# Kernel optimization log

Hardware: AMD Instinct MI355X
Metric: run time of the kernel (lower is better)

The kernel has to match this reference:

```python
import jax, jax.numpy as jnp
import numpy as np

B, C, H, W = 4, 256, 64, 64
HID = C // 2


def setup_inputs() -> dict:
    key = jax.random.key(0)
    kx, kp, kt, kg, km = jax.random.split(key, 5)
    return {
        "x": jax.random.normal(kx, (B, C, H, W), dtype=jnp.float32),
        "w_phi": jax.random.normal(kp, (HID, C), dtype=jnp.float32) * 0.02,
        "w_theta": jax.random.normal(kt, (HID, C), dtype=jnp.float32) * 0.02,
        "w_g": jax.random.normal(kg, (HID, C), dtype=jnp.float32) * 0.02,
        "w_mask": jax.random.normal(km, (C, HID), dtype=jnp.float32) * 0.02,
    }


def reference(x, w_phi, w_theta, w_g, w_mask):
    b, c, h, w = x.shape
    n = h * w
    xf = x.reshape(b, c, n)                     # [B,C,N]
    # 1x1 convs == channel GEMMs
    phi = jnp.einsum('oc,bcn->bon', w_phi, xf)      # [B,HID,N]
    theta = jnp.einsum('oc,bcn->bon', w_theta, xf)  # [B,HID,N]
    g = jnp.einsum('oc,bcn->bon', w_g, xf)          # [B,HID,N]
    # attn[b,n,m] = sum_c theta[b,c,n] * phi[b,c,m]   (theta^T @ phi)
    attn = jnp.einsum('bcn,bcm->bnm', theta, phi)   # [B,N,N]
    # Faithful to nn.Softmax(dim=1): normalize over axis 1 (theta index)
    attn = jax.nn.softmax(attn, axis=1)
    # attn_g[b,n,c] = sum_m attn[b,n,m] * g[b,c,m]   (attn @ g^T)
    attn_g = jnp.einsum('bnm,bcm->bcn', attn, g)    # [B,HID,N] (already transposed back)
    mask = jnp.einsum('oc,bcn->bon', w_mask, attn_g).reshape(b, c, h, w)
    return mask + x
```

## Files before the change

kernel.cpp:

```cpp
#include <hip/hip_runtime.h>


#define NB   4
#define CIN  256
#define HIDN 128
#define NPIX 4096

typedef __attribute__((ext_vector_type(8))) short short8;
typedef __attribute__((ext_vector_type(4))) float f32x4;
typedef __attribute__((ext_vector_type(16))) float f32x16;

__device__ __forceinline__ unsigned short f2bf(float f) {
    unsigned u = __builtin_bit_cast(unsigned, f);
    u += 0x7fffu + ((u >> 16) & 1u);
    return (unsigned short)(u >> 16);
}
__device__ __forceinline__ unsigned f2bf2(float lo, float hi) {
    return (unsigned)f2bf(lo) | ((unsigned)f2bf(hi) << 16);
}
__device__ __forceinline__ float bf2f(unsigned short s) {
    return __builtin_bit_cast(float, (unsigned)s << 16);
}
__device__ __forceinline__ void cp16(void* lds, const void* g) {
    __builtin_amdgcn_global_load_lds(
        (const __attribute__((address_space(1))) unsigned int*)g,
        (__attribute__((address_space(3))) unsigned int*)lds, 16, 0, 0);
}

__global__ __launch_bounds__(256) void k_proj(
    const float* __restrict__ x,
    const float* __restrict__ w_phi,
    const float* __restrict__ w_theta,
    const float* __restrict__ w_g,
    unsigned short* __restrict__ phiT,
    unsigned short* __restrict__ thetaT,
    unsigned short* __restrict__ gbuf)
{
    const int nt = blockIdx.x, p = blockIdx.y, b = blockIdx.z;
    const int n0 = nt * 128;
    const float* W = (p == 0) ? w_phi : (p == 1) ? w_theta : w_g;
    const float* X = x + (size_t)b * CIN * NPIX;

    __shared__ alignas(16) unsigned short Ws[128][40];
    __shared__ alignas(16) unsigned short Xs[128][40];

    const int tid = threadIdx.x;
    const int wave = tid >> 6, lane = tid & 63;
    const int wm = wave >> 1, wn = wave & 1;
    const int quad = lane >> 4, l16 = lane & 15;

    f32x4 acc[4][4];
#pragma unroll
    for (int i = 0; i < 4; ++i)
#pragma unroll
        for (int j = 0; j < 4; ++j) acc[i][j] = {0.f, 0.f, 0.f, 0.f};

    for (int ks = 0; ks < CIN / 32; ++ks) {
        {
            const int row = tid >> 1, c0 = (tid & 1) * 16;
            const float* src = W + (size_t)row * CIN + ks * 32 + c0;
            unsigned* dst = (unsigned*)&Ws[row][c0];
#pragma unroll
            for (int j = 0; j < 8; ++j) dst[j] = f2bf2(src[2 * j], src[2 * j + 1]);
        }
        {
            const int cp = (tid >> 4) * 2, nn0 = (tid & 15) * 8;
            const float* s0 = X + (size_t)(ks * 32 + cp) * NPIX + n0 + nn0;
            const float* s1 = s0 + NPIX;
#pragma unroll
            for (int j = 0; j < 8; ++j)
                *(unsigned*)&Xs[nn0 + j][cp] = f2bf2(s0[j], s1[j]);
        }
        __syncthreads();
#pragma unroll
        for (int mi = 0; mi < 4; ++mi) {
            short8 a = *(const short8*)&Ws[wm * 64 + mi * 16 + l16][quad * 8];
#pragma unroll
            for (int ni = 0; ni < 4; ++ni) {
                short8 bb = *(const short8*)&Xs[wn * 64 + ni * 16 + l16][quad * 8];
                acc[mi][ni] = __builtin_amdgcn_mfma_f32_16x16x32_bf16(a, bb, acc[mi][ni], 0, 0, 0);
            }
        }
        __syncthreads();
    }

    if (p < 2) {
        unsigned short* T = (p == 0) ? phiT : thetaT;
#pragma unroll
        for (int mi = 0; mi < 4; ++mi) {
            const int obase = wm * 64 + mi * 16 + quad * 4;
#pragma unroll
            for (int ni = 0; ni < 4; ++ni) {
                const int nn = wn * 64 + ni * 16 + l16;
                const int scol = (((obase >> 3) ^ (nn & 15)) << 3) | (obase & 7);
                uint2 v;
                v.x = f2bf2(acc[mi][ni][0], acc[mi][ni][1]);
                v.y = f2bf2(acc[mi][ni][2], acc[mi][ni][3]);
                *(uint2*)&T[((size_t)b * NPIX + n0 + nn) * HIDN + scol] = v;
            }
        }
    } else {
#pragma unroll
        for (int mi = 0; mi < 4; ++mi) {
            const int obase = wm * 64 + mi * 16 + quad * 4;
#pragma unroll
            for (int ni = 0; ni < 4; ++ni) {
                const int nn = wn * 64 + ni * 16 + l16;
#pragma unroll
                for (int r = 0; r < 4; ++r) {
                    const int c = obase + r;
                    const int scol = n0 + ((((nn >> 3) ^ (c & 15)) << 3) | (nn & 7));
                    gbuf[((size_t)b * HIDN + c) * NPIX + scol] = f2bf(acc[mi][ni][r]);
                }
            }
        }
    }
}

__global__ __launch_bounds__(256, 2) void k_colsum(
    const unsigned short* __restrict__ thetaT,
    const unsigned short* __restrict__ phiT,
    float* __restrict__ colsum)
{
    const int mt = blockIdx.x, ntg = blockIdx.y, b = blockIdx.z;
    const int m0 = mt * 128;
    __shared__ alignas(16) unsigned short As[128][128];
    __shared__ alignas(16) unsigned short Bs[128][128];
    const int tid = threadIdx.x;
    const int wave = tid >> 6, lane = tid & 63;
    const int wm = wave >> 1, wn = wave & 1;
    const int quad = lane >> 4, l16 = lane & 15;

    {
        const unsigned short* src = phiT + ((size_t)b * NPIX + m0) * HIDN;
#pragma unroll
        for (int i = 0; i < 8; ++i) {
            const int u = i * 256 + tid;
            cp16(&Bs[0][0] + u * 8, src + u * 8);
        }
    }

    float csum[4] = {0.f, 0.f, 0.f, 0.f};

    for (int nc = 0; nc < 4; ++nc) {
        const int n0 = ntg * 512 + nc * 128;
        __syncthreads();
        {
            const unsigned short* src = thetaT + ((size_t)b * NPIX + n0) * HIDN;
#pragma unroll
            for (int i = 0; i < 8; ++i) {
                const int u = i * 256 + tid;
                cp16(&As[0][0] + u * 8, src + u * 8);
            }
        }
        __syncthreads();

        f32x4 acc[4][4];
#pragma unroll
        for (int i = 0; i < 4; ++i)
#pragma unroll
            for (int j = 0; j < 4; ++j) acc[i][j] = {0.f, 0.f, 0.f, 0.f};

#pragma unroll
        for (int ks = 0; ks < 4; ++ks) {
            const int sc = (((ks * 4 + quad) ^ l16) << 3);
            short8 af[4], bf[4];
#pragma unroll
            for (int mi = 0; mi < 4; ++mi)
                af[mi] = *(const short8*)&As[wm * 64 + mi * 16 + l16][sc];
#pragma unroll
            for (int ni = 0; ni < 4; ++ni)
                bf[ni] = *(const short8*)&Bs[wn * 64 + ni * 16 + l16][sc];
#pragma unroll
            for (int mi = 0; mi < 4; ++mi)
#pragma unroll
                for (int ni = 0; ni < 4; ++ni)
                    acc[mi][ni] = __builtin_amdgcn_mfma_f32_16x16x32_bf16(af[mi], bf[ni], acc[mi][ni], 0, 0, 0);
        }
#pragma unroll
        for (int ni = 0; ni < 4; ++ni)
#pragma unroll
            for (int mi = 0; mi < 4; ++mi)
#pragma unroll
                for (int r = 0; r < 4; ++r) csum[ni] += __expf(acc[mi][ni][r]);
    }

#pragma unroll
    for (int ni = 0; ni < 4; ++ni) {
        float s = csum[ni];
        s += __shfl_xor(s, 16);
        s += __shfl_xor(s, 32);
        if (quad == 0)
            atomicAdd(&colsum[(size_t)b * NPIX + m0 + wn * 64 + ni * 16 + l16], s);
    }
}

__global__ void k_zero(float* __restrict__ p) { p[blockIdx.x * 256 + threadIdx.x] = 0.f; }
__global__ void k_zero4(float* __restrict__ p) {
    const size_t i = (size_t)(blockIdx.x * 256 + threadIdx.x) * 4;
    *(f32x4*)&p[i] = f32x4{0.f, 0.f, 0.f, 0.f};
}

__global__ __launch_bounds__(256) void k_scale_g(
    unsigned short* __restrict__ gbuf, const float* __restrict__ colsum)
{
    const int idx = blockIdx.x * 256 + threadIdx.x;
    const int row = idx >> 9;
    const int sc = (idx & 511) * 8;
    const int bb = row >> 7;
    const int mt = (sc & ~127) | ((((sc >> 3) & 15) ^ (row & 15)) << 3);
    uint4 v = *(uint4*)&gbuf[(size_t)row * NPIX + sc];
    float4 c0 = *(const float4*)&colsum[(size_t)bb * NPIX + mt];
    float4 c1 = *(const float4*)&colsum[(size_t)bb * NPIX + mt + 4];
    unsigned short* vs = (unsigned short*)&v;
    const float cs[8] = {c0.x, c0.y, c0.z, c0.w, c1.x, c1.y, c1.z, c1.w};
#pragma unroll
    for (int j = 0; j < 8; ++j) vs[j] = f2bf(bf2f(vs[j]) / cs[j]);
    *(uint4*)&gbuf[(size_t)row * NPIX + sc] = v;
}

__global__ __launch_bounds__(256, 2) void k_attn(
    const unsigned short* __restrict__ thetaT,
    const unsigned short* __restrict__ phiT,
    const unsigned short* __restrict__ gbuf,
    float* __restrict__ O32)
{
    const int nt = blockIdx.x, ms = blockIdx.y, b = blockIdx.z;
    const int n0 = nt * 64;

    __shared__ alignas(16) unsigned short Bs[128][128];
    __shared__ alignas(16) unsigned short Gs[128][128];
    __shared__ alignas(16) unsigned short Ps[64][128];

    const int tid = threadIdx.x;
    const int wave = tid >> 6, lane = tid & 63;
    const int wm = wave >> 1, wn = wave & 1;
    const int l31 = lane & 31, lh = lane >> 5;
    const int key = l31 & 15;

    short8 afrag[8];
    {
        const int n = n0 + wm * 32 + l31;
        const unsigned short* src = thetaT + ((size_t)b * NPIX + n) * HIDN;
#pragma unroll
        for (int ks = 0; ks < 8; ++ks)
            afrag[ks] = *(const short8*)(src + (((ks * 2 + lh) ^ key) << 3));
    }

    f32x16 accO[2];
#pragma unroll
    for (int r = 0; r < 16; ++r) { accO[0][r] = 0.f; accO[1][r] = 0.f; }

    for (int mc = 0; mc < 16; ++mc) {
        const int m0 = (ms * 16 + mc) * 128;
        __syncthreads();
        {
            const unsigned short* src = phiT + ((size_t)b * NPIX + m0) * HIDN;
#pragma unroll
            for (int i = 0; i < 8; ++i) {
                const int u = i * 256 + tid;
                cp16(&Bs[0][0] + u * 8, src + u * 8);
            }
        }
        {
#pragma unroll
            for (int i = 0; i < 8; ++i) {
                const int u = i * 256 + tid;
                const int row = u >> 4, un = u & 15;
                cp16(&Gs[0][0] + u * 8,
                     gbuf + ((size_t)b * HIDN + row) * NPIX + m0 + un * 8);
            }
        }
        __syncthreads();

        f32x16 accS[2];
#pragma unroll
        for (int r = 0; r < 16; ++r) { accS[0][r] = 0.f; accS[1][r] = 0.f; }
#pragma unroll
        for (int ks = 0; ks < 8; ++ks) {
            const int sc = ((ks * 2 + lh) ^ key) << 3;
            short8 b0 = *(const short8*)&Bs[wn * 64 + l31][sc];
            short8 b1 = *(const short8*)&Bs[wn * 64 + 32 + l31][sc];
            accS[0] = __builtin_amdgcn_mfma_f32_32x32x16_bf16(afrag[ks], b0, accS[0], 0, 0, 0);
            accS[1] = __builtin_amdgcn_mfma_f32_32x32x16_bf16(afrag[ks], b1, accS[1], 0, 0, 0);
        }
#pragma unroll
        for (int ni = 0; ni < 2; ++ni) {
            const int m_loc = wn * 64 + ni * 32 + l31;
#pragma unroll
            for (int r = 0; r < 16; ++r) {
                const int n_loc = wm * 32 + (r & 3) + 8 * (r >> 2) + 4 * lh;
                const int scol = (((m_loc >> 3) ^ (n_loc & 15)) << 3) | (m_loc & 7);
                Ps[n_loc][scol] = f2bf(__expf(accS[ni][r]));
            }
        }
        __syncthreads();
        {
            const int prow = wm * 32 + l31;
            const int pkey = prow & 15;
#pragma unroll
            for (int ks = 0; ks < 8; ++ks) {
                const int sc = ((ks * 2 + lh) ^ key) << 3;
                short8 pa = *(const short8*)&Ps[prow][((ks * 2 + lh) ^ pkey) << 3];
                short8 g0 = *(const short8*)&Gs[wn * 64 + l31][sc];
                short8 g1 = *(const short8*)&Gs[wn * 64 + 32 + l31][sc];
                accO[0] = __builtin_amdgcn_mfma_f32_32x32x16_bf16(pa, g0, accO[0], 0, 0, 0);
                accO[1] = __builtin_amdgcn_mfma_f32_32x32x16_bf16(pa, g1, accO[1], 0, 0, 0);
            }
        }
    }

#pragma unroll
    for (int ni = 0; ni < 2; ++ni)
#pragma unroll
        for (int r = 0; r < 16; ++r) {
            const int n = n0 + wm * 32 + (r & 3) + 8 * (r >> 2) + 4 * lh;
            const int c = wn * 64 + ni * 32 + l31;
            atomicAdd(&O32[((size_t)b * NPIX + n) * HIDN + c], accO[ni][r]);
        }
}

__global__ __launch_bounds__(256) void k_mask(
    const float* __restrict__ w_mask,
    const float* __restrict__ O32,
    const float* __restrict__ x,
    float* __restrict__ out)
{
    const int nt = blockIdx.x, ct = blockIdx.y, b = blockIdx.z;
    const int n0 = nt * 128, c0 = ct * 128;
    __shared__ alignas(16) unsigned short As[128][40];
    __shared__ alignas(16) unsigned short Bs[128][40];
    const int tid = threadIdx.x;
    const int wave = tid >> 6, lane = tid & 63;
    const int wm = wave >> 1, wn = wave & 1;
    const int quad = lane >> 4, l16 = lane & 15;

    f32x4 acc[4][4];
#pragma unroll
    for (int i = 0; i < 4; ++i)
#pragma unroll
        for (int j = 0; j < 4; ++j) acc[i][j] = {0.f, 0.f, 0.f, 0.f};

    for (int ks = 0; ks < 4; ++ks) {
        {
            const int row = tid >> 1, cc0 = (tid & 1) * 16;
            const float* src = w_mask + (size_t)(c0 + row) * HIDN + ks * 32 + cc0;
            unsigned* dst = (unsigned*)&As[row][cc0];
#pragma unroll
            for (int j = 0; j < 8; ++j) dst[j] = f2bf2(src[2 * j], src[2 * j + 1]);
        }
        {
            const int row = tid >> 1, h0 = (tid & 1) * 16;
            const float* src = O32 + ((size_t)b * NPIX + n0 + row) * HIDN + ks * 32 + h0;
            unsigned* dst = (unsigned*)&Bs[row][h0];
#pragma unroll
            for (int j = 0; j < 8; ++j) dst[j] = f2bf2(src[2 * j], src[2 * j + 1]);
        }
        __syncthreads();
#pragma unroll
        for (int mi = 0; mi < 4; ++mi) {
            short8 a = *(const short8*)&As[wm * 64 + mi * 16 + l16][quad * 8];
#pragma unroll
            for (int ni = 0; ni < 4; ++ni) {
                short8 bb = *(const short8*)&Bs[wn * 64 + ni * 16 + l16][quad * 8];
                acc[mi][ni] = __builtin_amdgcn_mfma_f32_16x16x32_bf16(a, bb, acc[mi][ni], 0, 0, 0);
            }
        }
        __syncthreads();
    }

#pragma unroll
    for (int mi = 0; mi < 4; ++mi)
#pragma unroll
        for (int ni = 0; ni < 4; ++ni)
#pragma unroll
            for (int r = 0; r < 4; ++r) {
                const int co = c0 + wm * 64 + mi * 16 + quad * 4 + r;
                const int nn = n0 + wn * 64 + ni * 16 + l16;
                const size_t idx = ((size_t)b * CIN + co) * NPIX + nn;
                out[idx] = acc[mi][ni][r] + x[idx];
            }
}

extern "C" void kernel_launch(void* const* d_in, const int* in_sizes, int n_in,
                              void* d_out, int out_size, void* d_ws, size_t ws_size,
                              hipStream_t stream)
{
    (void)in_sizes; (void)n_in; (void)out_size; (void)ws_size;
    const float* x       = (const float*)d_in[0];
    const float* w_phi   = (const float*)d_in[1];
    const float* w_theta = (const float*)d_in[2];
    const float* w_g     = (const float*)d_in[3];
    const float* w_mask  = (const float*)d_in[4];
    float* out = (float*)d_out;

    char* ws = (char*)d_ws;
    unsigned short* phiT   = (unsigned short*)(ws);
    unsigned short* thetaT = (unsigned short*)(ws + 4194304);
    unsigned short* gbuf   = (unsigned short*)(ws + 8388608);
    float*          colsum = (float*)(ws + 12582912);
    float*          O32    = (float*)(ws + 12648448);

    k_proj   <<<dim3(32, 3, 4), 256, 0, stream>>>(x, w_phi, w_theta, w_g, phiT, thetaT, gbuf);
    k_zero   <<<dim3(64),       256, 0, stream>>>(colsum);
    k_zero4  <<<dim3(2048),     256, 0, stream>>>(O32);
    k_colsum <<<dim3(32, 8, 4), 256, 0, stream>>>(thetaT, phiT, colsum);
    k_scale_g<<<dim3(1024),     256, 0, stream>>>(gbuf, colsum);
    k_attn   <<<dim3(64, 2, 4), 256, 0, stream>>>(thetaT, phiT, gbuf, O32);
    k_mask   <<<dim3(32, 2, 4), 256, 0, stream>>>(w_mask, O32, x, out);
}
```

Baseline: 186.5 us.

## Pre-convert weights and x to swizzled bf16, retile all GEMMs to 32x32 MFMA

Adds prep kernels that convert the weights and a transposed x to bf16 with XOR-swizzled layouts, so the projection and mask GEMMs can stream operands with direct global-to-LDS copies instead of converting fp32 element by element. Zeroing of colsum and O32 moves into the prep and colsum kernels, removing two launches. The projection, colsum, attention and mask kernels are retiled to 32x32x16 MFMA with smaller 64-wide tiles and higher occupancy hints, and attention now uses more blocks over the m dimension. The xT buffer shares workspace space with O32, which O32 only overwrites after xT is consumed. The trade-off is extra launches and global traffic for the prep step, plus more atomics into O32 from the wider split.

Measured after the change: 186.5 us. About the same (-0.0%).

```diff
diff --git a/kernel.cpp b/kernel.cpp
--- a/kernel.cpp
+++ b/kernel.cpp
@@ -27,178 +27,220 @@
         (__attribute__((address_space(3))) unsigned int*)lds, 16, 0, 0);
 }
 
-__global__ __launch_bounds__(256) void k_proj(
+__global__ __launch_bounds__(256) void k_prep_w(
+    const float* __restrict__ wp, const float* __restrict__ wt,
+    const float* __restrict__ wg, const float* __restrict__ wm,
+    unsigned short* __restrict__ Wp, unsigned short* __restrict__ Wt,
+    unsigned short* __restrict__ Wg, unsigned short* __restrict__ Wm)
+{
+    const int which = blockIdx.x >> 3;
+    const float* src = (which == 0) ? wp : (which == 1) ? wt : (which == 2) ? wg : wm;
+    unsigned short* dst = (which == 0) ? Wp : (which == 1) ? Wt : (which == 2) ? Wg : Wm;
+#pragma unroll
+    for (int t = 0; t < 2; ++t) {
+        const int gidx = ((blockIdx.x & 7) * 256 + threadIdx.x) * 2 + t;
+        int o, srcc, dstc;
+        if (which < 3) {
+            o = gidx >> 5;
+            const int gc = gidx & 31;
+            const int sg = (gc & ~15) | ((gc & 15) ^ (o & 15));
+            srcc = o * 256 + gc * 8; dstc = o * 256 + sg * 8;
+        } else {
+            o = gidx >> 4;
+            const int gc = gidx & 15;
+            const int sg = gc ^ (o & 15);
+            srcc = o * 128 + gc * 8; dstc = o * 128 + sg * 8;
+        }
+        float4 a = *(const float4*)&src[srcc];
+        float4 b = *(const float4*)&src[srcc + 4];
+        uint4 v;
+        v.x = f2bf2(a.x, a.y); v.y = f2bf2(a.z, a.w);
+        v.z = f2bf2(b.x, b.y); v.w = f2bf2(b.z, b.w);
+        *(uint4*)&dst[dstc] = v;
+    }
+}
+
+__global__ __launch_bounds__(256) void k_prep_x(
     const float* __restrict__ x,
-    const float* __restrict__ w_phi,
-    const float* __restrict__ w_theta,
-    const float* __restrict__ w_g,
+    unsigned short* __restrict__ xT,
+    float* __restrict__ colsum)
+{
+    const int nt = blockIdx.x, ct = blockIdx.y, b = blockIdx.z;
+    const int tid = threadIdx.x;
+    if (ct == 0 && tid < 64) colsum[(size_t)b * NPIX + nt * 64 + tid] = 0.f;
+
+    __shared__ unsigned short Ls[64][66];
+    {
+        const int c_loc = tid >> 2, n_seg = (tid & 3) * 16;
+        const float* src = x + ((size_t)(b * CIN + ct * 64 + c_loc)) * NPIX + nt * 64 + n_seg;
+#pragma unroll
+        for (int j = 0; j < 8; ++j)
+            *(unsigned*)&Ls[c_loc][n_seg + 2 * j] = f2bf2(src[2 * j], src[2 * j + 1]);
+    }
+    __syncthreads();
+    {
+        const int n_loc = tid >> 2, c_seg = (tid & 3) * 16;
+        const int n_glob = nt * 64 + n_loc;
+        unsigned short tmp[16];
+#pragma unroll
+        for (int j = 0; j < 16; ++j) tmp[j] = Ls[c_seg + j][n_loc];
+#pragma unroll
+        for (int gr = 0; gr < 2; ++gr) {
+            const int c_base = ct * 64 + c_seg + gr * 8;
+            const int sec = c_base >> 7;
+            const int sg = (((c_base >> 3) & 15) ^ (n_glob & 15));
+            *(uint4*)&xT[((size_t)b * NPIX + n_glob) * CIN + sec * 128 + sg * 8] =
+                *(uint4*)&tmp[gr * 8];
+        }
+    }
+}
+
+__global__ __launch_bounds__(256, 3) void k_proj(
+    const unsigned short* __restrict__ Wp,
+    const unsigned short* __restrict__ Wt,
+    const unsigned short* __restrict__ Wg,
+    const unsigned short* __restrict__ xT,
     unsigned short* __restrict__ phiT,
     unsigned short* __restrict__ thetaT,
     unsigned short* __restrict__ gbuf)
 {
-    const int nt = blockIdx.x, p = blockIdx.y, b = blockIdx.z;
-    const int n0 = nt * 128;
-    const float* W = (p == 0) ? w_phi : (p == 1) ? w_theta : w_g;
-    const float* X = x + (size_t)b * CIN * NPIX;
-
-    __shared__ alignas(16) unsigned short Ws[128][40];
-    __shared__ alignas(16) unsigned short Xs[128][40];
+    const int nt = blockIdx.x, ot = blockIdx.y, b = blockIdx.z;
+    const unsigned short* W = (ot == 0) ? Wp : (ot == 1) ? Wt : Wg;
+
+    __shared__ alignas(16) unsigned short Aw[128][128];
+    __shared__ alignas(16) unsigned short Bx[64][128];
 
     const int tid = threadIdx.x;
     const int wave = tid >> 6, lane = tid & 63;
-    const int wm = wave >> 1, wn = wave & 1;
-    const int quad = lane >> 4, l16 = lane & 15;
-
-    f32x4 acc[4][4];
-#pragma unroll
-    for (int i = 0; i < 4; ++i)
-#pragma unroll
-        for (int j = 0; j < 4; ++j) acc[i][j] = {0.f, 0.f, 0.f, 0.f};
-
-    for (int ks = 0; ks < CIN / 32; ++ks) {
-        {
-            const int row = tid >> 1, c0 = (tid & 1) * 16;
-            const float* src = W + (size_t)row * CIN + ks * 32 + c0;
-            unsigned* dst = (unsigned*)&Ws[row][c0];
-#pragma unroll
-            for (int j = 0; j < 8; ++j) dst[j] = f2bf2(src[2 * j], src[2 * j + 1]);
-        }
-        {
-            const int cp = (tid >> 4) * 2, nn0 = (tid & 15) * 8;
-            const float* s0 = X + (size_t)(ks * 32 + cp) * NPIX + n0 + nn0;
-            const float* s1 = s0 + NPIX;
-#pragma unroll
-            for (int j = 0; j < 8; ++j)
-                *(unsigned*)&Xs[nn0 + j][cp] = f2bf2(s0[j], s1[j]);
-        }
-        __syncthreads();
-#pragma unroll
-        for (int mi = 0; mi < 4; ++mi) {
-            short8 a = *(const short8*)&Ws[wm * 64 + mi * 16 + l16][quad * 8];
-#pragma unroll
-            for (int ni = 0; ni < 4; ++ni) {
-                short8 bb = *(const short8*)&Xs[wn * 64 + ni * 16 + l16][quad * 8];
-                acc[mi][ni] = __builtin_amdgcn_mfma_f32_16x16x32_bf16(a, bb, acc[mi][ni], 0, 0, 0);
+    const int oh = wave >> 1, nh = wave & 1;
+    const int l31 = lane & 31, lh = lane >> 5;
+    const int key = l31 & 15;
+
+    f32x16 acc[2];
+#pragma unroll
+    for (int r = 0; r < 16; ++r) { acc[0][r] = 0.f; acc[1][r] = 0.f; }
+
+    for (int kh = 0; kh < 2; ++kh) {
+        __syncthreads();
+#pragma unroll
+        for (int i = 0; i < 8; ++i) {
+            const int u = i * 256 + tid;
+            cp16(&Aw[0][0] + u * 8, W + (u >> 4) * 256 + kh * 128 + (u & 15) * 8);
+        }
+#pragma unroll
+        for (int i = 0; i < 4; ++i) {
+            const int u = i * 256 + tid;
+            cp16(&Bx[0][0] + u * 8,
+                 xT + ((size_t)b * NPIX + nt * 64 + (u >> 4)) * CIN + kh * 128 + (u & 15) * 8);
+        }
+        __syncthreads();
+#pragma unroll
+        for (int ks = 0; ks < 8; ++ks) {
+            const int g = ((ks * 2 + lh) ^ key) << 3;
+            short8 bb = *(const short8*)&Bx[nh * 32 + l31][g];
+#pragma unroll
+            for (int t = 0; t < 2; ++t) {
+                short8 a = *(const short8*)&Aw[oh * 64 + t * 32 + l31][g];
+                acc[t] = __builtin_amdgcn_mfma_f32_32x32x16_bf16(a, bb, acc[t], 0, 0, 0);
             }
         }
-        __syncthreads();
-    }
-
-    if (p < 2) {
-        unsigned short* T = (p == 0) ? phiT : thetaT;
-#pragma unroll
-        for (int mi = 0; mi < 4; ++mi) {
-            const int obase = wm * 64 + mi * 16 + quad * 4;
-#pragma unroll
-            for (int ni = 0; ni < 4; ++ni) {
-                const int nn = wn * 64 + ni * 16 + l16;
-                const int scol = (((obase >> 3) ^ (nn & 15)) << 3) | (obase & 7);
+    }
+
+    const int n_glob = nt * 64 + nh * 32 + l31;
+    if (ot < 2) {
+        unsigned short* T = (ot == 0) ? phiT : thetaT;
+#pragma unroll
+        for (int t = 0; t < 2; ++t)
+#pragma unroll
+            for (int rg = 0; rg < 4; ++rg) {
+                const int ob = oh * 64 + t * 32 + 8 * rg + 4 * lh;
+                const int sc = (((ob >> 3) ^ (n_glob & 15)) << 3) | (ob & 7);
                 uint2 v;
-                v.x = f2bf2(acc[mi][ni][0], acc[mi][ni][1]);
-                v.y = f2bf2(acc[mi][ni][2], acc[mi][ni][3]);
-                *(uint2*)&T[((size_t)b * NPIX + n0 + nn) * HIDN + scol] = v;
+                v.x = f2bf2(acc[t][rg * 4 + 0], acc[t][rg * 4 + 1]);
+                v.y = f2bf2(acc[t][rg * 4 + 2], acc[t][rg * 4 + 3]);
+                *(uint2*)&T[((size_t)b * NPIX + n_glob) * HIDN + sc] = v;
             }
-        }
     } else {
-#pragma unroll
-        for (int mi = 0; mi < 4; ++mi) {
-            const int obase = wm * 64 + mi * 16 + quad * 4;
-#pragma unroll
-            for (int ni = 0; ni < 4; ++ni) {
-                const int nn = wn * 64 + ni * 16 + l16;
-#pragma unroll
-                for (int r = 0; r < 4; ++r) {
-                    const int c = obase + r;
-                    const int scol = n0 + ((((nn >> 3) ^ (c & 15)) << 3) | (nn & 7));
-                    gbuf[((size_t)b * HIDN + c) * NPIX + scol] = f2bf(acc[mi][ni][r]);
-                }
+        const int sbase = n_glob & ~63;
+        const int g8 = (n_glob >> 3) & 7, c7off = n_glob & 7;
+#pragma unroll
+        for (int t = 0; t < 2; ++t)
+#pragma unroll
+            for (int r = 0; r < 16; ++r) {
+                const int c = oh * 64 + t * 32 + (r & 3) + 8 * (r >> 2) + 4 * lh;
+                const int sc = sbase | (((g8 ^ (c & 7)) << 3)) | c7off;
+                gbuf[((size_t)b * HIDN + c) * NPIX + sc] = f2bf(acc[t][r]);
             }
-        }
-    }
-}
-
-__global__ __launch_bounds__(256, 2) void k_colsum(
+    }
+}
+
+__global__ __launch_bounds__(256, 3) void k_colsum(
     const unsigned short* __restrict__ thetaT,
     const unsigned short* __restrict__ phiT,
-    float* __restrict__ colsum)
-{
-    const int mt = blockIdx.x, ntg = blockIdx.y, b = blockIdx.z;
-    const int m0 = mt * 128;
-    __shared__ alignas(16) unsigned short As[128][128];
-    __shared__ alignas(16) unsigned short Bs[128][128];
+    float* __restrict__ colsum,
+    float* __restrict__ O32)
+{
+    const int mt = blockIdx.x, ng = blockIdx.y, b = blockIdx.z;
     const int tid = threadIdx.x;
+    {
+        const int blin = ((blockIdx.z * 8 + blockIdx.y) * 32 + blockIdx.x);
+        float* p = O32 + (size_t)blin * 2048 + tid * 8;
+        *(f32x4*)p = f32x4{0.f, 0.f, 0.f, 0.f};
+        *(f32x4*)(p + 4) = f32x4{0.f, 0.f, 0.f, 0.f};
+    }
+
+    __shared__ alignas(16) unsigned short As[64][128];
+
     const int wave = tid >> 6, lane = tid & 63;
-    const int wm = wave >> 1, wn = wave & 1;
-    const int quad = lane >> 4, l16 = lane & 15;
-
-    {
-        const unsigned short* src = phiT + ((size_t)b * NPIX + m0) * HIDN;
-#pragma unroll
-        for (int i = 0; i < 8; ++i) {
+    const int wn = wave & 1, wh = wave >> 1;
+    const int l31 = lane & 31, lh = lane >> 5;
+    const int key = l31 & 15;
+
+    short8 bfrag[2][8];
+#pragma unroll
+    for (int t = 0; t < 2; ++t) {
+        const int m = mt * 128 + wn * 64 + t * 32 + l31;
+        const unsigned short* src = phiT + ((size_t)b * NPIX + m) * HIDN;
+#pragma unroll
+        for (int ks = 0; ks < 8; ++ks)
+            bfrag[t][ks] = *(const short8*)(src + (((ks * 2 + lh) ^ key) << 3));
+    }
+
+    float csum[2] = {0.f, 0.f};
+
+    for (int nc = 0; nc < 8; ++nc) {
+        const int n0 = ng * 512 + nc * 64;
+        __syncthreads();
+#pragma unroll
+        for (int i = 0; i < 4; ++i) {
             const int u = i * 256 + tid;
-            cp16(&Bs[0][0] + u * 8, src + u * 8);
-        }
-    }
-
-    float csum[4] = {0.f, 0.f, 0.f, 0.f};
-
-    for (int nc = 0; nc < 4; ++nc) {
-        const int n0 = ntg * 512 + nc * 128;
-        __syncthreads();
-        {
-            const unsigned short* src = thetaT + ((size_t)b * NPIX + n0) * HIDN;
-#pragma unroll
-            for (int i = 0; i < 8; ++i) {
-                const int u = i * 256 + tid;
-                cp16(&As[0][0] + u * 8, src + u * 8);
-            }
-        }
-        __syncthreads();
-
-        f32x4 acc[4][4];
-#pragma unroll
-        for (int i = 0; i < 4; ++i)
-#pragma unroll
-            for (int j = 0; j < 4; ++j) acc[i][j] = {0.f, 0.f, 0.f, 0.f};
-
-#pragma unroll
-        for (int ks = 0; ks < 4; ++ks) {
-            const int sc = (((ks * 4 + quad) ^ l16) << 3);
-            short8 af[4], bf[4];
-#pragma unroll
-            for (int mi = 0; mi < 4; ++mi)
-                af[mi] = *(const short8*)&As[wm * 64 + mi * 16 + l16][sc];
-#pragma unroll
-            for (int ni = 0; ni < 4; ++ni)
-                bf[ni] = *(const short8*)&Bs[wn * 64 + ni * 16 + l16][sc];
-#pragma unroll
-            for (int mi = 0; mi < 4; ++mi)
-#pragma unroll
-                for (int ni = 0; ni < 4; ++ni)
-                    acc[mi][ni] = __builtin_amdgcn_mfma_f32_16x16x32_bf16(af[mi], bf[ni], acc[mi][ni], 0, 0, 0);
-        }
-#pragma unroll
-        for (int ni = 0; ni < 4; ++ni)
-#pragma unroll
-            for (int mi = 0; mi < 4; ++mi)
-#pragma unroll
-                for (int r = 0; r < 4; ++r) csum[ni] += __expf(acc[mi][ni][r]);
-    }
-
-#pragma unroll
-    for (int ni = 0; ni < 4; ++ni) {
-        float s = csum[ni];
-        s += __shfl_xor(s, 16);
+            cp16(&As[0][0] + u * 8,
+                 thetaT + ((size_t)b * NPIX + n0 + (u >> 4)) * HIDN + (u & 15) * 8);
+        }
+        __syncthreads();
+
+        f32x16 acc[2];
+#pragma unroll
+        for (int r = 0; r < 16; ++r) { acc[0][r] = 0.f; acc[1][r] = 0.f; }
+#pragma unroll
+        for (int ks = 0; ks < 8; ++ks) {
+            short8 a = *(const short8*)&As[wh * 32 + l31][(((ks * 2 + lh) ^ key) << 3)];
+            acc[0] = __builtin_amdgcn_mfma_f32_32x32x16_bf16(a, bfrag[0][ks], acc[0], 0, 0, 0);
+            acc[1] = __builtin_amdgcn_mfma_f32_32x32x16_bf16(a, bfrag[1][ks], acc[1], 0, 0, 0);
+        }
+#pragma unroll
+        for (int t = 0; t < 2; ++t)
+#pragma unroll
+            for (int r = 0; r < 16; ++r) csum[t] += __expf(acc[t][r]);
+    }
+
+#pragma unroll
+    for (int t = 0; t < 2; ++t) {
+        float s = csum[t];
         s += __shfl_xor(s, 32);
-        if (quad == 0)
-            atomicAdd(&colsum[(size_t)b * NPIX + m0 + wn * 64 + ni * 16 + l16], s);
-    }
-}
-
-__global__ void k_zero(float* __restrict__ p) { p[blockIdx.x * 256 + threadIdx.x] = 0.f; }
-__global__ void k_zero4(float* __restrict__ p) {
-    const size_t i = (size_t)(blockIdx.x * 256 + threadIdx.x) * 4;
-    *(f32x4*)&p[i] = f32x4{0.f, 0.f, 0.f, 0.f};
+        if (lh == 0)
+            atomicAdd(&colsum[(size_t)b * NPIX + mt * 128 + wn * 64 + t * 32 + l31], s);
+    }
 }
 
 __global__ __launch_bounds__(256) void k_scale_g(
@@ -208,7 +250,7 @@
     const int row = idx >> 9;
     const int sc = (idx & 511) * 8;
     const int bb = row >> 7;
-    const int mt = (sc & ~127) | ((((sc >> 3) & 15) ^ (row & 15)) << 3);
+    const int mt = (sc & ~63) | (((((sc >> 3) & 7) ^ (row & 7))) << 3);
     uint4 v = *(uint4*)&gbuf[(size_t)row * NPIX + sc];
     float4 c0 = *(const float4*)&colsum[(size_t)bb * NPIX + mt];
     float4 c1 = *(const float4*)&colsum[(size_t)bb * NPIX + mt + 4];
@@ -219,7 +261,7 @@
     *(uint4*)&gbuf[(size_t)row * NPIX + sc] = v;
 }
 
-__global__ __launch_bounds__(256, 2) void k_attn(
+__global__ __launch_bounds__(256, 4) void k_attn(
     const unsigned short* __restrict__ thetaT,
     const unsigned short* __restrict__ phiT,
     const unsigned short* __restrict__ gbuf,
@@ -228,20 +270,19 @@
     const int nt = blockIdx.x, ms = blockIdx.y, b = blockIdx.z;
     const int n0 = nt * 64;
 
-    __shared__ alignas(16) unsigned short Bs[128][128];
-    __shared__ alignas(16) unsigned short Gs[128][128];
-    __shared__ alignas(16) unsigned short Ps[64][128];
+    __shared__ alignas(16) unsigned short Bs[64][128];
+    __shared__ alignas(16) unsigned short Gs[128][64];
+    __shared__ alignas(16) unsigned short Ps[64][64];
 
     const int tid = threadIdx.x;
     const int wave = tid >> 6, lane = tid & 63;
     const int wm = wave >> 1, wn = wave & 1;
     const int l31 = lane & 31, lh = lane >> 5;
-    const int key = l31 & 15;
+    const int key = l31 & 15, key7 = l31 & 7;
 
     short8 afrag[8];
     {
-        const int n = n0 + wm * 32 + l31;
-        const unsigned short* src = thetaT + ((size_t)b * NPIX + n) * HIDN;
+        const unsigned short* src = thetaT + ((size_t)b * NPIX + n0 + wm * 32 + l31) * HIDN;
 #pragma unroll
         for (int ks = 0; ks < 8; ++ks)
             afrag[ks] = *(const short8*)(src + (((ks * 2 + lh) ^ key) << 3));
@@ -252,134 +293,122 @@
     for (int r = 0; r < 16; ++r) { accO[0][r] = 0.f; accO[1][r] = 0.f; }
 
     for (int mc = 0; mc < 16; ++mc) {
-        const int m0 = (ms * 16 + mc) * 128;
-        __syncthreads();
+        const int m0 = (ms * 16 + mc) * 64;
+        __syncthreads();
+#pragma unroll
+        for (int i = 0; i < 4; ++i) {
+            const int u = i * 256 + tid;
+            cp16(&Bs[0][0] + u * 8,
+                 phiT + ((size_t)b * NPIX + m0 + (u >> 4)) * HIDN + (u & 15) * 8);
+        }
+#pragma unroll
+        for (int i = 0; i < 4; ++i) {
+            const int u = i * 256 + tid;
+            cp16(&Gs[0][0] + u * 8,
+                 gbuf + ((size_t)b * HIDN + (u >> 3)) * NPIX + m0 + (u & 7) * 8);
+        }
+        __syncthreads();
+
+        f32x16 accS;
+#pragma unroll
+        for (int r = 0; r < 16; ++r) accS[r] = 0.f;
+#pragma unroll
+        for (int ks = 0; ks < 8; ++ks) {
+            short8 bb = *(const short8*)&Bs[wn * 32 + l31][(((ks * 2 + lh) ^ key) << 3)];
+            accS = __builtin_amdgcn_mfma_f32_32x32x16_bf16(afrag[ks], bb, accS, 0, 0, 0);
+        }
         {
-            const unsigned short* src = phiT + ((size_t)b * NPIX + m0) * HIDN;
-#pragma unroll
-            for (int i = 0; i < 8; ++i) {
-                const int u = i * 256 + tid;
-                cp16(&Bs[0][0] + u * 8, src + u * 8);
-            }
-        }
-        {
-#pragma unroll
-            for (int i = 0; i < 8; ++i) {
-                const int u = i * 256 + tid;
-                const int row = u >> 4, un = u & 15;
-                cp16(&Gs[0][0] + u * 8,
-                     gbuf + ((size_t)b * HIDN + row) * NPIX + m0 + un * 8);
-            }
-        }
-        __syncthreads();
-
-        f32x16 accS[2];
-#pragma unroll
-        for (int r = 0; r < 16; ++r) { accS[0][r] = 0.f; accS[1][r] = 0.f; }
-#pragma unroll
-        for (int ks = 0; ks < 8; ++ks) {
-            const int sc = ((ks * 2 + lh) ^ key) << 3;
-            short8 b0 = *(const short8*)&Bs[wn * 64 + l31][sc];
-            short8 b1 = *(const short8*)&Bs[wn * 64 + 32 + l31][sc];
-            accS[0] = __builtin_amdgcn_mfma_f32_32x32x16_bf16(afrag[ks], b0, accS[0], 0, 0, 0);
-            accS[1] = __builtin_amdgcn_mfma_f32_32x32x16_bf16(afrag[ks], b1, accS[1], 0, 0, 0);
-        }
-#pragma unroll
-        for (int ni = 0; ni < 2; ++ni) {
-            const int m_loc = wn * 64 + ni * 32 + l31;
+            const int m_loc = wn * 32 + l31;
 #pragma unroll
             for (int r = 0; r < 16; ++r) {
                 const int n_loc = wm * 32 + (r & 3) + 8 * (r >> 2) + 4 * lh;
-                const int scol = (((m_loc >> 3) ^ (n_loc & 15)) << 3) | (m_loc & 7);
-                Ps[n_loc][scol] = f2bf(__expf(accS[ni][r]));
+                const int sc = (((m_loc >> 3) ^ (n_loc & 7)) << 3) | (m_loc & 7);
+                Ps[n_loc][sc] = f2bf(__expf(accS[r]));
             }
         }
         __syncthreads();
-        {
-            const int prow = wm * 32 + l31;
-            const int pkey = prow & 15;
-#pragma unroll
-            for (int ks = 0; ks < 8; ++ks) {
-                const int sc = ((ks * 2 + lh) ^ key) << 3;
-                short8 pa = *(const short8*)&Ps[prow][((ks * 2 + lh) ^ pkey) << 3];
-                short8 g0 = *(const short8*)&Gs[wn * 64 + l31][sc];
-                short8 g1 = *(const short8*)&Gs[wn * 64 + 32 + l31][sc];
-                accO[0] = __builtin_amdgcn_mfma_f32_32x32x16_bf16(pa, g0, accO[0], 0, 0, 0);
-                accO[1] = __builtin_amdgcn_mfma_f32_32x32x16_bf16(pa, g1, accO[1], 0, 0, 0);
-            }
-        }
-    }
-
-#pragma unroll
-    for (int ni = 0; ni < 2; ++ni)
+#pragma unroll
+        for (int ks = 0; ks < 4; ++ks) {
+            const int g = ((ks * 2 + lh) ^ key7) << 3;
+            short8 pa = *(const short8*)&Ps[wm * 32 + l31][g];
+            short8 g0 = *(const short8*)&Gs[wn * 64 + l31][g];
+            short8 g1 = *(const short8*)&Gs[wn * 64 + 32 + l31][g];
+            accO[0] = __builtin_amdgcn_mfma_f32_32x32x16_bf16(pa, g0, accO[0], 0, 0, 0);
+            accO[1] = __builtin_amdgcn_mfma_f32_32x32x16_bf16(pa, g1, accO[1], 0, 0, 0);
+        }
+    }
+
+#pragma unroll
+    for (int t = 0; t < 2; ++t)
 #pragma unroll
         for (int r = 0; r < 16; ++r) {
             const int n = n0 + wm * 32 + (r & 3) + 8 * (r >> 2) + 4 * lh;
-            const int c = wn * 64 + ni * 32 + l31;
-            atomicAdd(&O32[((size_t)b * NPIX + n) * HIDN + c], accO[ni][r]);
-        }
-}
-
-__global__ __launch_bounds__(256) void k_mask(
-    const float* __restrict__ w_mask,
+            const int c = wn * 64 + t * 32 + l31;
+            atomicAdd(&O32[((size_t)b * NPIX + n) * HIDN + c], accO[t][r]);
+        }
+}
+
+__global__ __launch_bounds__(256, 3) void k_mask(
+    const unsigned short* __restrict__ Wm,
     const float* __restrict__ O32,
     const float* __restrict__ x,
     float* __restrict__ out)
 {
     const int nt = blockIdx.x, ct = blockIdx.y, b = blockIdx.z;
-    const int n0 = nt * 128, c0 = ct * 128;
-    __shared__ alignas(16) unsigned short As[128][40];
-    __shared__ alignas(16) unsigned short Bs[128][40];
+    __shared__ alignas(16) unsigned short As[128][128];
+    __shared__ alignas(16) unsigned short Bs[64][128];
+
     const int tid = threadIdx.x;
     const int wave = tid >> 6, lane = tid & 63;
-    const int wm = wave >> 1, wn = wave & 1;
-    const int quad = lane >> 4, l16 = lane & 15;
-
-    f32x4 acc[4][4];
-#pragma unroll
-    for (int i = 0; i < 4; ++i)
-#pragma unroll
-        for (int j = 0; j < 4; ++j) acc[i][j] = {0.f, 0.f, 0.f, 0.f};
-
-    for (int ks = 0; ks < 4; ++ks) {
-        {
-            const int row = tid >> 1, cc0 = (tid & 1) * 16;
-            const float* src = w_mask + (size_t)(c0 + row) * HIDN + ks * 32 + cc0;
-            unsigned* dst = (unsigned*)&As[row][cc0];
-#pragma unroll
-            for (int j = 0; j < 8; ++j) dst[j] = f2bf2(src[2 * j], src[2 * j + 1]);
-        }
-        {
-            const int row = tid >> 1, h0 = (tid & 1) * 16;
-            const float* src = O32 + ((size_t)b * NPIX + n0 + row) * HIDN + ks * 32 + h0;
-            unsigned* dst = (unsigned*)&Bs[row][h0];
-#pragma unroll
-            for (int j = 0; j < 8; ++j) dst[j] = f2bf2(src[2 * j], src[2 * j + 1]);
-        }
-        __syncthreads();
-#pragma unroll
-        for (int mi = 0; mi < 4; ++mi) {
-            short8 a = *(const short8*)&As[wm * 64 + mi * 16 + l16][quad * 8];
-#pragma unroll
-            for (int ni = 0; ni < 4; ++ni) {
-                short8 bb = *(const short8*)&Bs[wn * 64 + ni * 16 + l16][quad * 8];
-                acc[mi][ni] = __builtin_amdgcn_mfma_f32_16x16x32_bf16(a, bb, acc[mi][ni], 0, 0, 0);
-            }
-        }
-        __syncthreads();
-    }
-
-#pragma unroll
-    for (int mi = 0; mi < 4; ++mi)
-#pragma unroll
-        for (int ni = 0; ni < 4; ++ni)
-#pragma unroll
-            for (int r = 0; r < 4; ++r) {
-                const int co = c0 + wm * 64 + mi * 16 + quad * 4 + r;
-                const int nn = n0 + wn * 64 + ni * 16 + l16;
-                const size_t idx = ((size_t)b * CIN + co) * NPIX + nn;
-                out[idx] = acc[mi][ni][r] + x[idx];
-            }
+    const int oh = wave >> 1, nh = wave & 1;
+    const int l31 = lane & 31, lh = lane >> 5;
+    const int key = l31 & 15;
+
+#pragma unroll
+    for (int i = 0; i < 8; ++i) {
+        const int u = i * 256 + tid;
+        cp16(&As[0][0] + u * 8, Wm + (ct * 128 + (u >> 4)) * HIDN + (u & 15) * 8);
+    }
+    {
+        const int n_loc = tid >> 2, seg = (tid & 3) * 32;
+        const float* src = O32 + ((size_t)b * NPIX + nt * 64 + n_loc) * HIDN + seg;
+        const int k7 = n_loc & 7;
+#pragma unroll
+        for (int j = 0; j < 4; ++j) {
+            const int gr = (seg >> 3) + j;
+            const int sg = (gr & ~7) | ((gr & 7) ^ k7);
+            const float* s8 = src + j * 8;
+            unsigned* d = (unsigned*)&Bs[n_loc][sg * 8];
+#pragma unroll
+            for (int k = 0; k < 4; ++k) d[k] = f2bf2(s8[2 * k], s8[2 * k + 1]);
+        }
+    }
+    __syncthreads();
+
+    f32x16 acc[2];
+#pragma unroll
+    for (int r = 0; r < 16; ++r) { acc[0][r] = 0.f; acc[1][r] = 0.f; }
+#pragma unroll
+    for (int ks = 0; ks < 8; ++ks) {
+        const int gr = ks * 2 + lh;
+        const int sgb = ((gr & ~7) | ((gr & 7) ^ (l31 & 7))) << 3;
+        short8 bb = *(const short8*)&Bs[nh * 32 + l31][sgb];
+#pragma unroll
+        for (int t = 0; t < 2; ++t) {
+            short8 a = *(const short8*)&As[oh * 64 + t * 32 + l31][((gr ^ key) << 3)];
+            acc[t] = __builtin_amdgcn_mfma_f32_32x32x16_bf16(a, bb, acc[t], 0, 0, 0);
+        }
+    }
+
+    const int n = nt * 64 + nh * 32 + l31;
+#pragma unroll
+    for (int t = 0; t < 2; ++t)
+#pragma unroll
+        for (int r = 0; r < 16; ++r) {
+            const int co = ct * 128 + oh * 64 + t * 32 + (r & 3) + 8 * (r >> 2) + 4 * lh;
+            const size_t idx = ((size_t)b * CIN + co) * NPIX + n;
+            out[idx] = acc[t][r] + x[idx];
+        }
 }
 
 extern "C" void kernel_launch(void* const* d_in, const int* in_sizes, int n_in,
@@ -399,13 +428,18 @@
     unsigned short* thetaT = (unsigned short*)(ws + 4194304);
     unsigned short* gbuf   = (unsigned short*)(ws + 8388608);
     float*          colsum = (float*)(ws + 12582912);
+    unsigned short* xT     = (unsigned short*)(ws + 12648448);
     float*          O32    = (float*)(ws + 12648448);
-
-    k_proj   <<<dim3(32, 3, 4), 256, 0, stream>>>(x, w_phi, w_theta, w_g, phiT, thetaT, gbuf);
-    k_zero   <<<dim3(64),       256, 0, stream>>>(colsum);
-    k_zero4  <<<dim3(2048),     256, 0, stream>>>(O32);
-    k_colsum <<<dim3(32, 8, 4), 256, 0, stream>>>(thetaT, phiT, colsum);
-    k_scale_g<<<dim3(1024),     256, 0, stream>>>(gbuf, colsum);
-    k_attn   <<<dim3(64, 2, 4), 256, 0, stream>>>(thetaT, phiT, gbuf, O32);
-    k_mask   <<<dim3(32, 2, 4), 256, 0, stream>>>(w_mask, O32, x, out);
-}
+    unsigned short* Wp     = (unsigned short*)(ws + 21037056);
+    unsigned short* Wt     = (unsigned short*)(ws + 21102592);
+    unsigned short* Wg     = (unsigned short*)(ws + 21168128);
+    unsigned short* Wm     = (unsigned short*)(ws + 21233664);
+
+    k_prep_w <<<dim3(32),        256, 0, stream>>>(w_phi, w_theta, w_g, w_mask, Wp, Wt, Wg, Wm);
+    k_prep_x <<<dim3(64, 4, 4),  256, 0, stream>>>(x, xT, colsum);
+    k_proj   <<<dim3(64, 3, 4),  256, 0, stream>>>(Wp, Wt, Wg, xT, phiT, thetaT, gbuf);
+    k_colsum <<<dim3(32, 8, 4),  256, 0, stream>>>(thetaT, phiT, colsum, O32);
+    k_scale_g<<<dim3(1024),      256, 0, stream>>>(gbuf, colsum);
+    k_attn   <<<dim3(64, 4, 4),  256, 0, stream>>>(thetaT, phiT, gbuf, O32);
+    k_mask   <<<dim3(64, 2, 4),  256, 0, stream>>>(Wm, O32, x, out);
+}
```
